# Optimization experiments

Measured on AMD Instinct MI355X. Metric: run time of the kernel, lower is better.

The kernel has to match this reference:

```python
import jax, jax.numpy as jnp
import numpy as np

B, N, V, K = 2, 4096, 32768, 128
BLUR = 0.05  # geomloss blur; eps = blur**p with p=2
# geomloss 'multiscale' eps-annealing: sigma from ~diameter down to blur with scaling=0.5,
# then a few extra iterations at the final eps.
SIGMAS = [2.0, 1.0, 0.5, 0.25, 0.125, 0.0625, BLUR]
EPS_LIST = [s * s for s in SIGMAS] + [BLUR * BLUR] * 5


def setup_inputs() -> dict:
    key = jax.random.key(0)
    k1, k2, k3, k4 = jax.random.split(key, 4)
    y_hat = jax.random.uniform(k1, (B, 3, V), dtype=jnp.float32)          # voxel densities
    xyz = jax.random.uniform(k2, (B, N, 3), dtype=jnp.float32)            # point positions
    w = jax.random.uniform(k3, (B, N, 3), dtype=jnp.float32)              # fx, fy, fz weights
    y = jnp.concatenate([xyz, w], axis=-1)                                # [B, N, 6]
    voxel_centers = jax.random.uniform(k4, (V, 3), dtype=jnp.float32)
    return {"y_hat": y_hat, "y": y, "voxel_centers": voxel_centers}


def _sqdist(x, y):
    # x: [B,n,3], y: [B,m,3] -> [B,n,m]
    xn = jnp.sum(x * x, axis=-1)
    yn = jnp.sum(y * y, axis=-1)
    d = xn[..., :, None] + yn[..., None, :] - 2.0 * jnp.einsum('bnd,bmd->bnm', x, y)
    return jnp.maximum(d, 0.0)


def _softmin(eps, C, h):
    # C: [B,n,m], h: [B,m] -> -eps * logsumexp_j(h_j - C_ij/eps): [B,n]
    return -eps * jax.nn.logsumexp(h[:, None, :] - C / eps, axis=-1)


def _loop_ab(a_log, b_log, C):
    # symmetric (averaged) Sinkhorn updates with eps annealing
    Ct = jnp.swapaxes(C, -1, -2)
    f = jnp.zeros(a_log.shape, C.dtype)
    g = jnp.zeros(b_log.shape, C.dtype)
    for eps in EPS_LIST:
        ft = _softmin(eps, C, b_log + g / eps)
        gt = _softmin(eps, Ct, a_log + f / eps)
        f, g = 0.5 * (f + ft), 0.5 * (g + gt)
    return f, g


def _loop_sym(a_log, C):
    # self-correlation (debiasing) potential: f = g by symmetry
    f = jnp.zeros(a_log.shape, C.dtype)
    for eps in EPS_LIST:
        f = 0.5 * (f + _softmin(eps, C, a_log + f / eps))
    return f


def _sinkhorn_div(a, x, b, y_pts, C_xx):
    # debiased Sinkhorn divergence S_eps(a,x ; b,y), p=2 cost C = |x-y|^2 / 2
    eps = EPS_LIST[-1]
    a_log = jnp.log(jnp.maximum(a, 1e-20))
    b_log = jnp.log(jnp.maximum(b, 1e-20))
    C_xy = 0.5 * _sqdist(x, y_pts)        # [B,N,K]
    C_yy = 0.5 * _sqdist(y_pts, y_pts)    # [B,K,K]
    # run annealed iterations without grad (geomloss envelope-theorem style),
    # then one final differentiable update
    f0, g0 = jax.lax.stop_gradient(_loop_ab(a_log, b_log, C_xy))
    fa0 = jax.lax.stop_gradient(_loop_sym(a_log, C_xx))
    gb0 = jax.lax.stop_gradient(_loop_sym(b_log, C_yy))
    F_ab = _softmin(eps, C_xy, b_log + g0 / eps)
    G_ab = _softmin(eps, jnp.swapaxes(C_xy, -1, -2), a_log + f0 / eps)
    F_a = _softmin(eps, C_xx, a_log + fa0 / eps)
    G_b = _softmin(eps, C_yy, b_log + gb0 / eps)
    return jnp.sum(a * (F_ab - F_a), axis=-1) + jnp.sum(b * (G_ab - G_b), axis=-1)


def reference(y_hat, y, voxel_centers):
    xyz = y[:, :, :3]                                   # [B,N,3]
    yh = y_hat.reshape(y_hat.shape[0], y_hat.shape[1], -1)  # [B,3,V]
    C_xx = 0.5 * _sqdist(xyz, xyz)                      # [B,N,N] shared self-cost
    total = jnp.zeros((), xyz.dtype)
    for c in range(3):
        w = y[:, :, 3 + c]                              # [B,N] weights (fx/fy/fz)
        vals, idx = jax.lax.top_k(yh[:, c], K)          # [B,K] top-K voxel densities
        pts = voxel_centers[idx]                        # [B,K,3] gathered centers
        total = total + jnp.sum(_sinkhorn_div(w, xyz, vals, pts, C_xx))
    return total
```

## Files before the change

### kernel.cpp

```cpp
#include <hip/hip_runtime.h>
#include <math.h>

#define B_   2
#define N_   4096
#define V_   32768
#define K_   128
#define SC   16
#define CH   3
#define NEPS 12
#define XXB  256
#define FTB  96
#define GTB  192
#define YYB  6
#define NBLK (XXB + FTB + GTB + YYB)
#define TCAP 4096

#define LOG2E 1.4426950408889634f
#define LN2   0.6931471805599453f
#define EPS_LAST 0.0025f

typedef float f2 __attribute__((ext_vector_type(2)));

__device__ __forceinline__ float fexp2(float x) {
  float r; asm("v_exp_f32 %0, %1" : "=v"(r) : "v"(x)); return r;
}
__device__ __forceinline__ float flog2(float x) {
  float r; asm("v_log_f32 %0, %1" : "=v"(r) : "v"(x)); return r;
}

__device__ float4 g_P   [B_*N_];
__device__ float  g_alog[B_*CH*N_];
__device__ float  g_fa  [2][B_*CH*N_];
__device__ float  g_partS[2][SC*CH*B_*N_];
__device__ float  g_Ubar[2][B_*SC*CH];
__device__ float4 g_pts [B_*CH*K_];
__device__ float  g_blog[B_*CH*K_];
__device__ float  g_bval[B_*CH*K_];
__device__ float  g_fbuf[2][B_*CH*N_];
__device__ float  g_gbuf[2][B_*CH*K_];
__device__ float  g_ybuf[2][B_*CH*K_];
__device__ float  g_S1a[FTB];
__device__ float  g_Gab[768];
__device__ float  g_S2[6];
__device__ float  g_S3[96];
__device__ int    g_hist[6*32768];
__device__ int    g_bstar[6];
__device__ int    g_c1[6];
__device__ int    g_wcnt[6];
__device__ int    g_tcnt[6];
__device__ float  g_wval[6*K_];
__device__ int    g_widx[6*K_];
__device__ float  g_tval[6*TCAP];
__device__ int    g_tidx[6*TCAP];

__device__ __forceinline__ void lse_up(float t, float& m, float& s) {
  float mn = fmaxf(m, t);
  float e  = fexp2(-fabsf(t - m));
  bool  gt = t > m;
  float mulv = gt ? e : 1.0f;
  float addv = gt ? 1.0f : e;
  s = fmaf(s, mulv, addv);
  m = mn;
}
__device__ __forceinline__ void lse_merge(float& M, float& S, float oM, float oS) {
  float mn = fmaxf(M, oM);
  float e  = fexp2(-fabsf(M - oM));
  bool  gt = oM > M;
  float sm = gt ? e : 1.0f;
  float so = gt ? 1.0f : e;
  S = fmaf(S, sm, oS * so);
  M = mn;
}

__global__ __launch_bounds__(1024) void k_prep(const float* __restrict__ y) {
  const int blk = blockIdx.x, tid = threadIdx.x;
  const int gid = blk * 1024 + tid;
  g_hist[gid] = 0; g_hist[gid + 65536] = 0; g_hist[gid + 131072] = 0;
  if (blk == 62 && tid < 6) { g_wcnt[tid] = 0; g_tcnt[tid] = 0; }
  if (blk == 63 && tid < 768) { g_gbuf[0][tid] = 0.f; g_ybuf[0][tid] = 0.f; }
  if (blk < 8) {
    const int bn = gid;
    const int b = bn >> 12, n = bn & (N_ - 1);
    const float* yr = y + (size_t)bn * 6;
    float x0 = yr[0], x1 = yr[1], x2 = yr[2];
    g_P[bn] = make_float4(x0, x1, x2, 0.5f * (x0*x0 + x1*x1 + x2*x2));
#pragma unroll
    for (int c = 0; c < CH; ++c) {
      float w  = yr[3 + c];
      float al = flog2(fmaxf(w, 1e-20f)) * LN2;
      const int o = (b*CH + c)*N_ + n;
      g_alog[o] = al; g_fa[0][o] = 0.f; g_fbuf[0][o] = 0.f;
    }
  }
}

__global__ __launch_bounds__(1024) void k_topk1(const float* __restrict__ yhat) {
  const int bc = blockIdx.x >> 3, sub = blockIdx.x & 7, tid = threadIdx.x;
  const float* row = yhat + (size_t)bc * V_;
#pragma unroll
  for (int j = 0; j < 4; ++j) {
    int i = sub * 4096 + j * 1024 + tid;
    unsigned bk = __float_as_uint(row[i]) >> 15;
    atomicAdd(&g_hist[bc * 32768 + bk], 1);
  }
}

__global__ __launch_bounds__(1024) void k_topk3(const float* __restrict__ yhat) {
  const int bc = blockIdx.x >> 3, sub = blockIdx.x & 7, tid = threadIdx.x;
  const int* hist = g_hist + bc * 32768;
  __shared__ int s_suf[1024];
  __shared__ int s_bs;
  const int base = tid * 32;
  int cs = 0;
#pragma unroll 8
  for (int i = 0; i < 32; ++i) cs += hist[base + i];
  s_suf[tid] = cs;
  __syncthreads();
  for (int off = 1; off < 1024; off <<= 1) {
    int v = s_suf[tid];
    int add = (tid + off < 1024) ? s_suf[tid + off] : 0;
    __syncthreads();
    s_suf[tid] = v + add;
    __syncthreads();
  }
  int nxt = (tid < 1023) ? s_suf[tid + 1] : 0;
  if (s_suf[tid] >= K_ && nxt < K_) {
    int cnt = nxt, bstar = base, c1 = nxt;
    for (int b = base + 31; b >= base; --b) {
      int h = hist[b];
      if (cnt + h >= K_) { bstar = b; c1 = cnt; break; }
      cnt += h;
    }
    s_bs = bstar;
    g_bstar[bc] = bstar; g_c1[bc] = c1;
  }
  __syncthreads();
  const int bstar = s_bs;
  const float* row = yhat + (size_t)bc * V_;
#pragma unroll
  for (int j = 0; j < 4; ++j) {
    int i = sub * 4096 + j * 1024 + tid;
    float v = row[i];
    int bk = (int)(__float_as_uint(v) >> 15);
    if (bk > bstar) {
      int p = atomicAdd(&g_wcnt[bc], 1);
      g_wval[bc*K_ + p] = v; g_widx[bc*K_ + p] = i;
    } else if (bk == bstar) {
      int p = atomicAdd(&g_tcnt[bc], 1);
      if (p < TCAP) { g_tval[bc*TCAP + p] = v; g_tidx[bc*TCAP + p] = i; }
    }
  }
}

__global__ __launch_bounds__(1024) void k_topk4(const float* __restrict__ yhat,
                                                const float* __restrict__ vox) {
  const int bc = blockIdx.x, tid = threadIdx.x;
  __shared__ float s_tv[TCAP]; __shared__ int s_ti[TCAP];
  __shared__ float s_wv[K_];   __shared__ int s_wi[K_];
  __shared__ int s_wtot[16];
  __shared__ int s_cnt;
  const int c1 = g_c1[bc];
  const int tcnt = g_tcnt[bc];
  for (int e = tid; e < c1; e += 1024) { s_wv[e] = g_wval[bc*K_+e]; s_wi[e] = g_widx[bc*K_+e]; }
  if (tcnt <= TCAP) {
    const int need = K_ - c1;
    for (int e = tid; e < tcnt; e += 1024) { s_tv[e] = g_tval[bc*TCAP+e]; s_ti[e] = g_tidx[bc*TCAP+e]; }
    __syncthreads();
    for (int e = tid; e < tcnt; e += 1024) {
      float v = s_tv[e]; int i = s_ti[e];
      int rank = 0;
      for (int j = 0; j < tcnt; ++j) {
        float ov = s_tv[j]; int oi = s_ti[j];
        rank += (ov > v || (ov == v && oi < i)) ? 1 : 0;
      }
      if (rank < need) { s_wv[c1 + rank] = v; s_wi[c1 + rank] = i; }
    }
    __syncthreads();
  } else {
    const float* row = yhat + (size_t)bc * V_;
    float v[32];
#pragma unroll
    for (int j = 0; j < 32; ++j) v[j] = row[tid + j * 1024];
    unsigned lo = 0u, hi = 0x7f800000u;
    while (lo < hi) {
      unsigned mid = lo + ((hi - lo + 1u) >> 1);
      if (tid == 0) s_cnt = 0;
      __syncthreads();
      int local = 0;
#pragma unroll
      for (int j = 0; j < 32; ++j) local += (__float_as_uint(v[j]) >= mid) ? 1 : 0;
      for (int off = 32; off; off >>= 1) local += __shfl_down(local, off);
      if ((tid & 63) == 0 && local) atomicAdd(&s_cnt, local);
      __syncthreads();
      int cnt = s_cnt;
      __syncthreads();
      if (cnt >= K_) lo = mid; else hi = mid - 1u;
    }
    const unsigned T = lo;
    if (tid == 0) s_cnt = 0;
    __syncthreads();
#pragma unroll
    for (int j = 0; j < 32; ++j) {
      if (__float_as_uint(v[j]) > T) {
        int p = atomicAdd(&s_cnt, 1);
        s_wv[p] = v[j]; s_wi[p] = tid + j * 1024;
      }
    }
    __syncthreads();
    int got = s_cnt;
    __syncthreads();
    for (int chunk = 0; chunk < 32 && got < K_; ++chunk) {
      int i = chunk * 1024 + tid;
      bool f = (__float_as_uint(v[chunk]) == T);
      unsigned long long mask = __ballot(f);
      int lane = tid & 63, wv = tid >> 6;
      int wpre = __popcll(mask & ((1ULL << lane) - 1ULL));
      if (lane == 0) s_wtot[wv] = __popcll(mask);
      __syncthreads();
      int pre = wpre, tot = 0;
      for (int w = 0; w < 16; ++w) { if (w < wv) pre += s_wtot[w]; tot += s_wtot[w]; }
      if (f && got + pre < K_) { s_wv[got + pre] = v[chunk]; s_wi[got + pre] = i; }
      got = min(got + tot, K_);
      __syncthreads();
    }
  }
  if (tid < K_) {
    float mv = s_wv[tid]; int mi = s_wi[tid];
    float p0 = vox[(size_t)mi*3+0], p1 = vox[(size_t)mi*3+1], p2 = vox[(size_t)mi*3+2];
    g_pts [bc*K_ + tid] = make_float4(p0, p1, p2, 0.5f*(p0*p0 + p1*p1 + p2*p2));
    g_bval[bc*K_ + tid] = mv;
    g_blog[bc*K_ + tid] = flog2(fmaxf(mv, 1e-20f)) * LN2;
  }
}

__global__ __launch_bounds__(256) void k_pass(float eps, float eps_prev, int it, int mode,
                                              const float* __restrict__ y) {
  const float il = LOG2E / eps, nil = -il;
  const int blk = blockIdx.x, tid = threadIdx.x;
  const int src = it & 1;
  __shared__ float s_M[2048];
  __shared__ float s_scale[48];
  __shared__ float s_Mx[3];
  __shared__ float s_w[12];

  if (blk < XXB) {
    const int J = blk & 15;
    const int I = (blk >> 4) & 7;
    const int b = blk >> 7;
    const int r  = (J << 8) + tid;
    const int bn_r = b*N_ + r;
    float U[CH];
    if (it == 0) {
#pragma unroll
      for (int c = 0; c < CH; ++c) U[c] = LOG2E * g_alog[(b*CH + c)*N_ + r];
    } else {
      const int pv = src ^ 1;
      if (tid < 48) {
        int c = tid >> 4, Jp = tid & 15;
        s_scale[tid] = g_Ubar[pv][(b*SC + Jp)*CH + c];
      }
      __syncthreads();
      if (tid < 3) {
        float mm = s_scale[tid*16];
#pragma unroll
        for (int j = 1; j < 16; ++j) mm = fmaxf(mm, s_scale[tid*16 + j]);
        s_Mx[tid] = mm;
      }
      __syncthreads();
      if (tid < 48) s_scale[tid] = fexp2(s_scale[tid] - s_Mx[tid >> 4]);
      __syncthreads();
#pragma unroll
      for (int c = 0; c < CH; ++c) {
        float S = 0.f;
#pragma unroll
        for (int Jp = 0; Jp < 16; ++Jp)
          S = fmaf(g_partS[pv][(Jp*CH + c)*(B_*N_) + bn_r], s_scale[c*16 + Jp], S);
        float sm = -eps_prev * LN2 * (s_Mx[c] + flog2(S));
        const int o = (b*CH + c)*N_ + r;
        float fn = 0.5f * (g_fa[src ^ 1][o] + sm);
        g_fa[src][o] = fn;
        U[c] = fmaf(fn, il, LOG2E * g_alog[o]);
      }
      __syncthreads();
    }
    float Ub[CH];
#pragma unroll
    for (int c = 0; c < CH; ++c) {
      float u = U[c];
      for (int off = 32; off; off >>= 1) u = fmaxf(u, __shfl_xor(u, off));
      if ((tid & 63) == 0) s_w[(tid >> 6)*3 + c] = u;
    }
    __syncthreads();
#pragma unroll
    for (int c = 0; c < CH; ++c)
      Ub[c] = fmaxf(fmaxf(s_w[c], s_w[3 + c]), fmaxf(s_w[6 + c], s_w[9 + c]));
    if (tid < 3) g_Ubar[src][(b*SC + J)*CH + tid] = Ub[tid];
    {
      float4 Pm = g_P[bn_r];
      const int pp = tid >> 1, par = tid & 1;
      float* rec = s_M + pp*16;
      rec[0 + par] = il * Pm.x;
      rec[2 + par] = il * Pm.y;
      rec[4 + par] = il * Pm.z;
      rec[6 + par] = -il * Pm.w;
#pragma unroll
      for (int c = 0; c < CH; ++c) rec[8 + 2*c + par] = fexp2(U[c] - Ub[c]);
    }
    __syncthreads();
    const int bn0 = b*N_ + (I << 9) + tid;
    const int bn1 = bn0 + 256;
    const float4 Pn0 = g_P[bn0], Pn1 = g_P[bn1];
    const float xs0 = Pn0.x, ys0 = Pn0.y, zs0 = Pn0.z, nn0 = nil * Pn0.w;
    const float xs1 = Pn1.x, ys1 = Pn1.y, zs1 = Pn1.z, nn1 = nil * Pn1.w;
    const f2 zz = {0.f, 0.f};
    f2 a00 = zz, a01 = zz, a02 = zz, a10 = zz, a11 = zz, a12 = zz;
    for (int j = 0; j < 128; ++j) {
      const float* Mj = s_M + j*16;
      const float4 q0 = *(const float4*)(Mj);
      const float4 q1 = *(const float4*)(Mj + 4);
      const float4 q2 = *(const float4*)(Mj + 8);
      const float2 q3 = *(const float2*)(Mj + 12);
      f2 t0 = f2{q1.z, q1.w} + nn0;
      t0 = f2{q1.x, q1.y} * zs0 + t0;
      t0 = f2{q0.z, q0.w} * ys0 + t0;
      t0 = f2{q0.x, q0.y} * xs0 + t0;
      t0 = __builtin_elementwise_min(t0, zz);
      f2 e0; e0.x = fexp2(t0.x); e0.y = fexp2(t0.y);
      a00 = f2{q2.x, q2.y} * e0 + a00;
      a01 = f2{q2.z, q2.w} * e0 + a01;
      a02 = f2{q3.x, q3.y} * e0 + a02;
      f2 t1 = f2{q1.z, q1.w} + nn1;
      t1 = f2{q1.x, q1.y} * zs1 + t1;
      t1 = f2{q0.z, q0.w} * ys1 + t1;
      t1 = f2{q0.x, q0.y} * xs1 + t1;
      t1 = __builtin_elementwise_min(t1, zz);
      f2 e1; e1.x = fexp2(t1.x); e1.y = fexp2(t1.y);
      a10 = f2{q2.x, q2.y} * e1 + a10;
      a11 = f2{q2.z, q2.w} * e1 + a11;
      a12 = f2{q3.x, q3.y} * e1 + a12;
    }
    float* pc = g_partS[src];
    pc[(J*CH + 0)*(B_*N_) + bn0] = a00.x + a00.y;
    pc[(J*CH + 1)*(B_*N_) + bn0] = a01.x + a01.y;
    pc[(J*CH + 2)*(B_*N_) + bn0] = a02.x + a02.y;
    pc[(J*CH + 0)*(B_*N_) + bn1] = a10.x + a10.y;
    pc[(J*CH + 1)*(B_*N_) + bn1] = a11.x + a11.y;
    pc[(J*CH + 2)*(B_*N_) + bn1] = a12.x + a12.y;
  } else if (blk < XXB + FTB) {
    float4* s_A = (float4*)s_M;
    float*  s_C = s_M + 512;
    float*  s_D = s_M + 640;
    const int blk2 = blk - XXB;
    const int bc = blk2 >> 4;
    const int b = bc / 3, c = bc % 3;
    const int n = ((blk2 & 15) << 8) + tid;
    float Hk = -INFINITY;
    if (tid < K_) {
      float g = g_gbuf[src][bc*K_ + tid];
      Hk = fmaf(g, il, LOG2E * g_blog[bc*K_ + tid]);
      s_A[tid] = g_pts[bc*K_ + tid];
    }
    float hm = Hk;
    for (int off = 32; off; off >>= 1) hm = fmaxf(hm, __shfl_xor(hm, off));
    if ((tid & 63) == 0) s_w[tid >> 6] = hm;
    __syncthreads();
    const float Hbar = fmaxf(fmaxf(s_w[0], s_w[1]), fmaxf(s_w[2], s_w[3]));
    if (tid < K_) { float dh = Hk - Hbar; s_C[tid] = fexp2(dh); s_D[tid] = dh; }
    float4 Pn = g_P[b*N_ + n];
    __syncthreads();
    float S = 0.f, T = 0.f, M = -INFINITY;
#pragma unroll 4
    for (int k2 = 0; k2 < K_; k2 += 2) {
      float4 p1 = s_A[k2];
      float d1 = fmaf(Pn.x, p1.x, fmaf(Pn.y, p1.y, Pn.z * p1.z));
      float C1 = fmaxf((Pn.w + p1.w) - d1, 0.f);
      float w1 = C1 * nil;
      S = fmaf(s_C[k2], fexp2(w1), S);
      M = fmaxf(M, w1 + s_D[k2]);
      float4 p2 = s_A[k2+1];
      float d2 = fmaf(Pn.x, p2.x, fmaf(Pn.y, p2.y, Pn.z * p2.z));
      float C2 = fmaxf((Pn.w + p2.w) - d2, 0.f);
      float w2 = C2 * nil;
      T = fmaf(s_C[k2+1], fexp2(w2), T);
      M = fmaxf(M, w2 + s_D[k2+1]);
    }
    S += T;
    float lse = (S > 0.f) ? flog2(S) : M;
    float ft = -eps * LN2 * (Hbar + lse);
    if (mode == 0) {
      g_fbuf[src ^ 1][bc*N_ + n] = 0.5f * (g_fbuf[src][bc*N_ + n] + ft);
    } else {
      float a = y[(size_t)(b*N_ + n) * 6 + 3 + c];
      float acc = a * ft;
      for (int off = 32; off; off >>= 1) acc += __shfl_down(acc, off);
      __syncthreads();
      if ((tid & 63) == 0) s_w[tid >> 6] = acc;
      __syncthreads();
      if (tid == 0) g_S1a[blk2] = s_w[0] + s_w[1] + s_w[2] + s_w[3];
    }
  } else if (blk < XXB + FTB + GTB) {
    const int job = (blk - (XXB + FTB)) * 4 + (tid >> 6);
    const int bc = job >> 7, k = job & (K_ - 1);
    const int b = bc / 3;
    const int lane = tid & 63;
    float4 Pk = g_pts[bc*K_ + k];
    float M0=-INFINITY,S0=0.f,M1=-INFINITY,S1=0.f,M2=-INFINITY,S2=0.f,M3=-INFINITY,S3=0.f;
    for (int j = 0; j < 64; j += 4) {
#pragma unroll
      for (int u = 0; u < 4; ++u) {
        int n = ((j + u) << 6) + lane;
        float4 pm = g_P[b*N_ + n];
        float Hn = fmaf(g_fbuf[src][bc*N_ + n], il, LOG2E * g_alog[bc*N_ + n]);
        float d = fmaf(Pk.x, pm.x, fmaf(Pk.y, pm.y, Pk.z * pm.z));
        float C = fmaxf((Pk.w + pm.w) - d, 0.f);
        float t = fmaf(C, nil, Hn);
        if (u == 0) lse_up(t, M0, S0);
        else if (u == 1) lse_up(t, M1, S1);
        else if (u == 2) lse_up(t, M2, S2);
        else lse_up(t, M3, S3);
      }
    }
    lse_merge(M0, S0, M1, S1);
    lse_merge(M2, S2, M3, S3);
    lse_merge(M0, S0, M2, S2);
    for (int off = 1; off < 64; off <<= 1) {
      float oM = __shfl_xor(M0, off);
      float oS = __shfl_xor(S0, off);
      lse_merge(M0, S0, oM, oS);
    }
    if (lane == 0) {
      float gt = -eps * LN2 * (M0 + flog2(S0));
      const int o = bc*K_ + k;
      if (mode == 0) g_gbuf[src ^ 1][o] = 0.5f * (g_gbuf[src][o] + gt);
      else           g_Gab[job] = g_bval[o] * gt;
    }
  } else {
    float4* s_A = (float4*)s_M;
    float*  s_C = s_M + 512;
    float*  s_D = s_M + 640;
    const int bc = blk - (XXB + FTB + GTB);
    const int k = tid & (K_ - 1);
    if (tid < K_) {
      s_A[tid] = g_pts[bc*K_ + tid];
      float g = g_ybuf[src][bc*K_ + tid];
      s_C[tid] = fmaf(g, il, LOG2E * g_blog[bc*K_ + tid]);
      s_D[tid] = g;
    }
    __syncthreads();
    float4 Pk = s_A[k];
    float M = -INFINITY, S = 0.f;
    for (int m = 0; m < K_; ++m) {
      float4 pm = s_A[m];
      float d = fmaf(Pk.x, pm.x, fmaf(Pk.y, pm.y, Pk.z * pm.z));
      float C = fmaxf((Pk.w + pm.w) - d, 0.f);
      lse_up(fmaf(C, nil, s_C[m]), M, S);
    }
    float sv = -eps * LN2 * (M + flog2(S));
    if (mode == 0) {
      if (tid < K_) g_ybuf[src ^ 1][bc*K_ + k] = 0.5f * (s_D[k] + sv);
    } else {
      float val = (tid < K_) ? g_bval[bc*K_ + k] * sv : 0.f;
      for (int off = 32; off; off >>= 1) val += __shfl_down(val, off);
      __syncthreads();
      if ((tid & 63) == 0) s_w[tid >> 6] = val;
      __syncthreads();
      if (tid == 0) g_S2[bc] = s_w[0] + s_w[1] + s_w[2] + s_w[3];
    }
  }
}

__global__ __launch_bounds__(256) void k_finalize(const float* __restrict__ y) {
  const int tid = threadIdx.x;
  const int idx = blockIdx.x * 256 + tid;
  const int c  = idx >> 13;
  const int bn = idx & (B_*N_ - 1);
  const int b = bn >> 12, n = bn & (N_ - 1);
  __shared__ float s_scale[SC];
  __shared__ float s_mm;
  __shared__ float s_w[4];
  if (tid < SC) s_scale[tid] = g_Ubar[0][(b*SC + tid)*CH + c];
  __syncthreads();
  if (tid == 0) {
    float mm = s_scale[0];
#pragma unroll
    for (int s = 1; s < SC; ++s) mm = fmaxf(mm, s_scale[s]);
    s_mm = mm;
  }
  __syncthreads();
  const float Mmax = s_mm;
  if (tid < SC) s_scale[tid] = fexp2(s_scale[tid] - Mmax);
  __syncthreads();
  float S = 0.f;
#pragma unroll
  for (int s = 0; s < SC; ++s)
    S = fmaf(g_partS[0][(s*CH + c)*(B_*N_) + bn], s_scale[s], S);
  float sm = -EPS_LAST * LN2 * (Mmax + flog2(S));
  float a = y[(size_t)(b*N_ + n)*6 + 3 + c];
  float acc = a * sm;
  for (int off = 32; off; off >>= 1) acc += __shfl_down(acc, off);
  if ((tid & 63) == 0) s_w[tid >> 6] = acc;
  __syncthreads();
  if (tid == 0) g_S3[blockIdx.x] = s_w[0] + s_w[1] + s_w[2] + s_w[3];
}

__global__ __launch_bounds__(1024) void k_total(float* __restrict__ out) {
  const int tid = threadIdx.x;
  float local = 0.f;
  if (tid < 768) local += g_Gab[tid];
  if (tid < FTB) local += g_S1a[tid];
  if (tid < 96)  local -= g_S3[tid];
  if (tid < 6)   local -= g_S2[tid];
  for (int off = 32; off; off >>= 1) local += __shfl_down(local, off);
  __shared__ float s_red[16];
  if ((tid & 63) == 0) s_red[tid >> 6] = local;
  __syncthreads();
  if (tid == 0) {
    float t = 0.f;
#pragma unroll
    for (int i = 0; i < 16; ++i) t += s_red[i];
    out[0] = t;
  }
}

extern "C" void kernel_launch(void* const* d_in, const int* in_sizes, int n_in,
                              void* d_out, int out_size, void* d_ws, size_t ws_size,
                              hipStream_t stream) {
  const float* y_hat = (const float*)d_in[0];
  const float* y     = (const float*)d_in[1];
  const float* vox   = (const float*)d_in[2];
  float* out = (float*)d_out;

  static const float eps_list[NEPS + 1] = {4.0f, 1.0f, 0.25f, 0.0625f, 0.015625f, 0.00390625f,
                                           0.0025f, 0.0025f, 0.0025f, 0.0025f, 0.0025f, 0.0025f,
                                           EPS_LAST};

  k_prep<<<64, 1024, 0, stream>>>(y);
  k_topk1<<<48, 1024, 0, stream>>>(y_hat);
  k_topk3<<<48, 1024, 0, stream>>>(y_hat);
  k_topk4<<<6, 1024, 0, stream>>>(y_hat, vox);
  for (int it = 0; it <= NEPS; ++it) {
    float eps_prev = (it > 0) ? eps_list[it - 1] : 1.0f;
    int mode = (it == NEPS) ? 1 : 0;
    k_pass<<<NBLK, 256, 0, stream>>>(eps_list[it], eps_prev, it, mode, y);
  }
  k_finalize<<<96, 256, 0, stream>>>(y);
  k_total<<<1, 1024, 0, stream>>>(out);
}
```

Measured before the change: 283.8 us.

## Fuse top-k histogram, threshold and selection into one shared-memory kernel

Replaces the three global-memory top-k kernels (global histogram, threshold scan, tie ranking) with one kernel per (batch, channel) row. It builds an 8192-bin histogram in shared memory and keeps the row values in registers. This removes the global histogram clearing, the global atomics and two kernel launches. The trade-off is coarser buckets, which put more values in the tie bucket and lower its capacity, so the quadratic tie ranking or the binary-search fallback may run more often. Only 6 blocks now do the whole top-k stage, so the stage has little parallelism.

```diff
diff --git a/kernel.cpp b/kernel.cpp
--- a/kernel.cpp
+++ b/kernel.cpp
@@ -13,7 +13,7 @@
 #define GTB  192
 #define YYB  6
 #define NBLK (XXB + FTB + GTB + YYB)
-#define TCAP 4096
+#define TCAP 2048
 
 #define LOG2E 1.4426950408889634f
 #define LN2   0.6931471805599453f
@@ -43,15 +43,6 @@
 __device__ float  g_Gab[768];
 __device__ float  g_S2[6];
 __device__ float  g_S3[96];
-__device__ int    g_hist[6*32768];
-__device__ int    g_bstar[6];
-__device__ int    g_c1[6];
-__device__ int    g_wcnt[6];
-__device__ int    g_tcnt[6];
-__device__ float  g_wval[6*K_];
-__device__ int    g_widx[6*K_];
-__device__ float  g_tval[6*TCAP];
-__device__ int    g_tidx[6*TCAP];
 
 __device__ __forceinline__ void lse_up(float t, float& m, float& s) {
   float mn = fmaxf(m, t);
@@ -73,114 +64,102 @@
 }
 
 __global__ __launch_bounds__(1024) void k_prep(const float* __restrict__ y) {
-  const int blk = blockIdx.x, tid = threadIdx.x;
-  const int gid = blk * 1024 + tid;
-  g_hist[gid] = 0; g_hist[gid + 65536] = 0; g_hist[gid + 131072] = 0;
-  if (blk == 62 && tid < 6) { g_wcnt[tid] = 0; g_tcnt[tid] = 0; }
-  if (blk == 63 && tid < 768) { g_gbuf[0][tid] = 0.f; g_ybuf[0][tid] = 0.f; }
-  if (blk < 8) {
-    const int bn = gid;
-    const int b = bn >> 12, n = bn & (N_ - 1);
-    const float* yr = y + (size_t)bn * 6;
-    float x0 = yr[0], x1 = yr[1], x2 = yr[2];
-    g_P[bn] = make_float4(x0, x1, x2, 0.5f * (x0*x0 + x1*x1 + x2*x2));
-#pragma unroll
-    for (int c = 0; c < CH; ++c) {
-      float w  = yr[3 + c];
-      float al = flog2(fmaxf(w, 1e-20f)) * LN2;
-      const int o = (b*CH + c)*N_ + n;
-      g_alog[o] = al; g_fa[0][o] = 0.f; g_fbuf[0][o] = 0.f;
-    }
-  }
-}
-
-__global__ __launch_bounds__(1024) void k_topk1(const float* __restrict__ yhat) {
-  const int bc = blockIdx.x >> 3, sub = blockIdx.x & 7, tid = threadIdx.x;
+  const int bn = blockIdx.x * 1024 + threadIdx.x;
+  const int b = bn >> 12, n = bn & (N_ - 1);
+  const float* yr = y + (size_t)bn * 6;
+  float x0 = yr[0], x1 = yr[1], x2 = yr[2];
+  g_P[bn] = make_float4(x0, x1, x2, 0.5f * (x0*x0 + x1*x1 + x2*x2));
+#pragma unroll
+  for (int c = 0; c < CH; ++c) {
+    float w  = yr[3 + c];
+    float al = flog2(fmaxf(w, 1e-20f)) * LN2;
+    const int o = (b*CH + c)*N_ + n;
+    g_alog[o] = al; g_fa[0][o] = 0.f; g_fbuf[0][o] = 0.f;
+  }
+}
+
+__global__ __launch_bounds__(1024) void k_topk(const float* __restrict__ yhat,
+                                               const float* __restrict__ vox) {
+  const int bc = blockIdx.x, tid = threadIdx.x;
+  __shared__ int   s_hist[8192];
+  __shared__ int   s_suf[1024];
+  __shared__ float s_tv[TCAP];
+  __shared__ int   s_ti[TCAP];
+  __shared__ float s_wv[K_];
+  __shared__ int   s_wi[K_];
+  __shared__ int   s_wtot[16];
+  __shared__ int   s_pos, s_eq, s_bs, s_c1, s_cnt;
+
+  if (tid < K_) { g_gbuf[0][bc*K_ + tid] = 0.f; g_ybuf[0][bc*K_ + tid] = 0.f; }
+#pragma unroll
+  for (int j = 0; j < 8; ++j) s_hist[tid + j*1024] = 0;
+  if (tid == 0) { s_pos = 0; s_eq = 0; }
+
   const float* row = yhat + (size_t)bc * V_;
-#pragma unroll
-  for (int j = 0; j < 4; ++j) {
-    int i = sub * 4096 + j * 1024 + tid;
-    unsigned bk = __float_as_uint(row[i]) >> 15;
-    atomicAdd(&g_hist[bc * 32768 + bk], 1);
-  }
-}
-
-__global__ __launch_bounds__(1024) void k_topk3(const float* __restrict__ yhat) {
-  const int bc = blockIdx.x >> 3, sub = blockIdx.x & 7, tid = threadIdx.x;
-  const int* hist = g_hist + bc * 32768;
-  __shared__ int s_suf[1024];
-  __shared__ int s_bs;
-  const int base = tid * 32;
+  float v[32];
+#pragma unroll
+  for (int j = 0; j < 32; ++j) v[j] = row[tid + j * 1024];
+  __syncthreads();
+#pragma unroll
+  for (int j = 0; j < 32; ++j) {
+    unsigned b = __float_as_uint(v[j]);
+    unsigned bk = (b >> 31) ? 0u : min(b >> 17, 8191u);
+    atomicAdd(&s_hist[bk], 1);
+  }
+  __syncthreads();
+  const int base = tid * 8;
   int cs = 0;
-#pragma unroll 8
-  for (int i = 0; i < 32; ++i) cs += hist[base + i];
+#pragma unroll
+  for (int i = 0; i < 8; ++i) cs += s_hist[base + i];
   s_suf[tid] = cs;
   __syncthreads();
   for (int off = 1; off < 1024; off <<= 1) {
-    int v = s_suf[tid];
+    int vv = s_suf[tid];
     int add = (tid + off < 1024) ? s_suf[tid + off] : 0;
     __syncthreads();
-    s_suf[tid] = v + add;
+    s_suf[tid] = vv + add;
     __syncthreads();
   }
   int nxt = (tid < 1023) ? s_suf[tid + 1] : 0;
   if (s_suf[tid] >= K_ && nxt < K_) {
     int cnt = nxt, bstar = base, c1 = nxt;
-    for (int b = base + 31; b >= base; --b) {
-      int h = hist[b];
-      if (cnt + h >= K_) { bstar = b; c1 = cnt; break; }
+    for (int b2 = base + 7; b2 >= base; --b2) {
+      int h = s_hist[b2];
+      if (cnt + h >= K_) { bstar = b2; c1 = cnt; break; }
       cnt += h;
     }
-    s_bs = bstar;
-    g_bstar[bc] = bstar; g_c1[bc] = c1;
-  }
-  __syncthreads();
-  const int bstar = s_bs;
-  const float* row = yhat + (size_t)bc * V_;
-#pragma unroll
-  for (int j = 0; j < 4; ++j) {
-    int i = sub * 4096 + j * 1024 + tid;
-    float v = row[i];
-    int bk = (int)(__float_as_uint(v) >> 15);
+    s_bs = bstar; s_c1 = c1;
+  }
+  __syncthreads();
+  const int bstar = s_bs, c1 = s_c1;
+#pragma unroll
+  for (int j = 0; j < 32; ++j) {
+    unsigned b = __float_as_uint(v[j]);
+    int bk = (b >> 31) ? 0 : (int)min(b >> 17, 8191u);
+    int i = tid + j * 1024;
     if (bk > bstar) {
-      int p = atomicAdd(&g_wcnt[bc], 1);
-      g_wval[bc*K_ + p] = v; g_widx[bc*K_ + p] = i;
+      int p = atomicAdd(&s_pos, 1);
+      s_wv[p] = v[j]; s_wi[p] = i;
     } else if (bk == bstar) {
-      int p = atomicAdd(&g_tcnt[bc], 1);
-      if (p < TCAP) { g_tval[bc*TCAP + p] = v; g_tidx[bc*TCAP + p] = i; }
-    }
-  }
-}
-
-__global__ __launch_bounds__(1024) void k_topk4(const float* __restrict__ yhat,
-                                                const float* __restrict__ vox) {
-  const int bc = blockIdx.x, tid = threadIdx.x;
-  __shared__ float s_tv[TCAP]; __shared__ int s_ti[TCAP];
-  __shared__ float s_wv[K_];   __shared__ int s_wi[K_];
-  __shared__ int s_wtot[16];
-  __shared__ int s_cnt;
-  const int c1 = g_c1[bc];
-  const int tcnt = g_tcnt[bc];
-  for (int e = tid; e < c1; e += 1024) { s_wv[e] = g_wval[bc*K_+e]; s_wi[e] = g_widx[bc*K_+e]; }
+      int p = atomicAdd(&s_eq, 1);
+      if (p < TCAP) { s_tv[p] = v[j]; s_ti[p] = i; }
+    }
+  }
+  __syncthreads();
+  const int tcnt = s_eq;
   if (tcnt <= TCAP) {
     const int need = K_ - c1;
-    for (int e = tid; e < tcnt; e += 1024) { s_tv[e] = g_tval[bc*TCAP+e]; s_ti[e] = g_tidx[bc*TCAP+e]; }
-    __syncthreads();
     for (int e = tid; e < tcnt; e += 1024) {
-      float v = s_tv[e]; int i = s_ti[e];
+      float vv = s_tv[e]; int i = s_ti[e];
       int rank = 0;
-      for (int j = 0; j < tcnt; ++j) {
-        float ov = s_tv[j]; int oi = s_ti[j];
-        rank += (ov > v || (ov == v && oi < i)) ? 1 : 0;
+      for (int j2 = 0; j2 < tcnt; ++j2) {
+        float ov = s_tv[j2]; int oi = s_ti[j2];
+        rank += (ov > vv || (ov == vv && oi < i)) ? 1 : 0;
       }
-      if (rank < need) { s_wv[c1 + rank] = v; s_wi[c1 + rank] = i; }
+      if (rank < need) { s_wv[c1 + rank] = vv; s_wi[c1 + rank] = i; }
     }
     __syncthreads();
   } else {
-    const float* row = yhat + (size_t)bc * V_;
-    float v[32];
-#pragma unroll
-    for (int j = 0; j < 32; ++j) v[j] = row[tid + j * 1024];
     unsigned lo = 0u, hi = 0x7f800000u;
     while (lo < hi) {
       unsigned mid = lo + ((hi - lo + 1u) >> 1);
@@ -534,10 +513,8 @@
                                            0.0025f, 0.0025f, 0.0025f, 0.0025f, 0.0025f, 0.0025f,
                                            EPS_LAST};
 
-  k_prep<<<64, 1024, 0, stream>>>(y);
-  k_topk1<<<48, 1024, 0, stream>>>(y_hat);
-  k_topk3<<<48, 1024, 0, stream>>>(y_hat);
-  k_topk4<<<6, 1024, 0, stream>>>(y_hat, vox);
+  k_prep<<<8, 1024, 0, stream>>>(y);
+  k_topk<<<6, 1024, 0, stream>>>(y_hat, vox);
   for (int it = 0; it <= NEPS; ++it) {
     float eps_prev = (it > 0) ? eps_list[it - 1] : 1.0f;
     int mode = (it == NEPS) ? 1 : 0;
```

Result: faster. 250.6 us, median of 2 (-11.7%).
